# Optimization experiments

Measured on AMD Instinct MI355X. Metric: run time of the kernel, lower is better.

## Reference

```python
import jax, jax.numpy as jnp
import numpy as np

H, C, DK = 4, 63, 64   # n_head, context_size, d_k
NF = H * DK            # n_feat = 256


def setup_inputs() -> dict:
    key = jax.random.key(0)
    ks = jax.random.split(key, 7)
    B, T = 2, 4096
    query = jax.random.normal(ks[0], (B, T, NF), jnp.float32)
    key_t = jax.random.normal(ks[1], (B, T, NF), jnp.float32)   # dummy, unused
    value = jax.random.normal(ks[2], (B, T, NF), jnp.float32)
    mask = jnp.ones((B, 1, T), jnp.bool_)                       # dummy, unused
    s = 1.0 / np.sqrt(NF).astype(np.float32)
    w1 = jax.random.normal(ks[3], (NF, NF), jnp.float32) * s
    w2 = jax.random.normal(ks[4], (H * C, NF), jnp.float32) * s
    w3 = jax.random.normal(ks[5], (NF, NF), jnp.float32) * s
    w_out = jax.random.normal(ks[6], (NF, NF), jnp.float32) * s
    return {"query": query, "key": key_t, "value": value, "mask": mask,
            "w1": w1, "w2": w2, "w3": w3, "w_out": w_out}


def reference(query, key, value, mask, w1, w2, w3, w_out):
    # key and mask are dummies (unused), matching the original module.
    B, T, _ = query.shape
    half = (C - 1) // 2

    q = query @ w1.T                                            # (B,T,NF)
    # synthesized band scores: (B,H,T,C)
    weight = (jax.nn.relu(q) @ w2.T).reshape(B, T, H, C).transpose(0, 2, 1, 3)

    # band geometry: score(i, j) lives at offset k = j - i + half, |j-i| <= half
    j_idx = jnp.arange(T)[:, None] + jnp.arange(C)[None, :] - half   # (T,C)
    valid = (j_idx >= 0) & (j_idx < T)                               # (T,C)
    scores = jnp.where(valid[None, None], weight, -jnp.inf)
    p_attn = jax.nn.softmax(scores, axis=-1)                         # (B,H,T,C)

    v = (value @ w3.T).reshape(B, T, H, DK).transpose(0, 2, 1, 3)    # (B,H,T,DK)
    jc = jnp.clip(j_idx, 0, T - 1)                                   # safe gather idx
    windows = v[:, :, jc, :]                                         # (B,H,T,C,DK)
    x = jnp.einsum('bhtc,bhtcd->bhtd', p_attn, windows)              # (B,H,T,DK)

    x = x.transpose(0, 2, 1, 3).reshape(B, T, NF)
    return x @ w_out.T
```

## Files before the change

### kernel.cpp

```cpp
#include <hip/hip_runtime.h>
#include <hip/hip_bf16.h>
#include <math.h>

typedef _Float16 f16x8 __attribute__((ext_vector_type(8)));
typedef _Float16 f16x4 __attribute__((ext_vector_type(4)));
typedef float    f32x4 __attribute__((ext_vector_type(4)));

__device__ __host__ __forceinline__ int swz(int ch, int row) {
    return (ch & 24) | ((ch & 7) ^ (row & 7));
}
__device__ __forceinline__ f32x4 mfma16(f16x8 a, f16x8 b, f32x4 c) {
    return __builtin_amdgcn_mfma_f32_16x16x32_f16(a, b, c, 0, 0, 0);
}
__device__ __forceinline__ f16x8 cvt8(float4 lo, float4 hi) {
    f16x8 r = { (_Float16)lo.x, (_Float16)lo.y, (_Float16)lo.z, (_Float16)lo.w,
                (_Float16)hi.x, (_Float16)hi.y, (_Float16)hi.z, (_Float16)hi.w };
    return r;
}

__global__ __launch_bounds__(256) void convw(const float* __restrict__ w1,
                                             const float* __restrict__ w2,
                                             const float* __restrict__ w3,
                                             const float* __restrict__ wo,
                                             _Float16* __restrict__ p1,
                                             _Float16* __restrict__ p2,
                                             _Float16* __restrict__ p3,
                                             _Float16* __restrict__ po) {
    int gid = blockIdx.x * 256 + threadIdx.x;
    int widx = gid >> 13;
    int r    = gid & 8191;
    int lane = r & 63;
    int ks   = (r >> 6) & 7;
    int nblk = r >> 9;
    int n  = nblk * 16 + (lane & 15);
    int kc = (ks * 4 + (lane >> 4)) * 8;
    const float* src = widx == 0 ? w1 : widx == 1 ? w2 : widx == 2 ? w3 : wo;
    _Float16*    dst = widx == 0 ? p1 : widx == 1 ? p2 : widx == 2 ? p3 : po;
    f16x8 h = {};
    if (!(widx == 1 && n >= 252)) {
        float4 lo = *(const float4*)&src[n * 256 + kc];
        float4 hi = *(const float4*)&src[n * 256 + kc + 4];
        h = cvt8(lo, hi);
    }
    *(f16x8*)&dst[r * 8] = h;
}

__global__ __launch_bounds__(512, 2) void mono(const float* __restrict__ query,
                                               const float* __restrict__ value,
                                               const _Float16* __restrict__ w1p,
                                               const _Float16* __restrict__ w2p,
                                               const _Float16* __restrict__ w3p,
                                               const _Float16* __restrict__ wop,
                                               float* __restrict__ outp) {
    __shared__ __align__(16) _Float16 RA[16384];
    __shared__ __align__(16) _Float16 RB[8192];
    __shared__ __align__(16) _Float16 Vs[24576];
    __shared__ __align__(16) _Float16 vwT[26624];

    const int tid = threadIdx.x, lane = tid & 63, wid = tid >> 6;
    const int bidr = blockIdx.x;
    const int work = (bidr & 7) * 32 + (bidr >> 3);
    const int b   = work >> 7;
    const int t0  = (work & 127) * 32;
    const size_t rowb = (size_t)b * 4096;

    _Float16* Aq = RA;
    _Float16* Qr = RA + 8192;
    _Float16* Pl = RA;
    _Float16* sc = RB;
    _Float16* xb = RB;

    #pragma unroll
    for (int it = 0; it < 2; ++it) {
        int slot = it * 512 + tid;
        int row = slot >> 5, ch = slot & 31;
        const float* p = &query[(rowb + t0 + row) * 256 + ch * 8];
        float4 lo = *(const float4*)p, hi = *(const float4*)(p + 4);
        *(f16x8*)&Aq[row * 256 + swz(ch, row) * 8] = cvt8(lo, hi);
    }
    #pragma unroll
    for (int it = 0; it < 6; ++it) {
        int slot = it * 512 + tid;
        int row = slot >> 5, ch = slot & 31;
        int jl = t0 - 32 + row;
        jl = jl < 0 ? 0 : (jl > 4095 ? 4095 : jl);
        const float* p = &value[(rowb + jl) * 256 + ch * 8];
        float4 lo = *(const float4*)p, hi = *(const float4*)(p + 4);
        *(f16x8*)&Vs[row * 256 + swz(ch, row) * 8] = cvt8(lo, hi);
    }
    __syncthreads();

    {
        f32x4 acc[2][2] = {};
        #pragma unroll
        for (int ks = 0; ks < 8; ++ks) {
            int chn = ks * 4 + (lane >> 4);
            f16x8 af[2], bf[2];
            #pragma unroll
            for (int i = 0; i < 2; ++i) {
                int row = i * 16 + (lane & 15);
                af[i] = *(const f16x8*)&Aq[row * 256 + swz(chn, row) * 8];
            }
            #pragma unroll
            for (int j = 0; j < 2; ++j)
                bf[j] = *(const f16x8*)&w1p[(((wid * 2 + j) * 8 + ks) * 64 + lane) * 8];
            #pragma unroll
            for (int i = 0; i < 2; ++i)
                #pragma unroll
                for (int j = 0; j < 2; ++j)
                    acc[i][j] = mfma16(af[i], bf[j], acc[i][j]);
        }
        #pragma unroll
        for (int i = 0; i < 2; ++i)
            #pragma unroll
            for (int j = 0; j < 2; ++j)
                #pragma unroll
                for (int r = 0; r < 4; ++r) {
                    int row = i * 16 + ((lane >> 4) << 2) + r;
                    int n   = wid * 32 + j * 16 + (lane & 15);
                    float v = fmaxf(acc[i][j][r], 0.f);
                    Qr[row * 256 + swz(n >> 3, row) * 8 + (n & 7)] = (_Float16)v;
                }
    }
    __syncthreads();

    {
        f32x4 acc[2][2] = {};
        #pragma unroll
        for (int ks = 0; ks < 8; ++ks) {
            int chn = ks * 4 + (lane >> 4);
            f16x8 af[2], bf[2];
            #pragma unroll
            for (int i = 0; i < 2; ++i) {
                int row = i * 16 + (lane & 15);
                af[i] = *(const f16x8*)&Qr[row * 256 + swz(chn, row) * 8];
            }
            #pragma unroll
            for (int j = 0; j < 2; ++j)
                bf[j] = *(const f16x8*)&w2p[(((wid * 2 + j) * 8 + ks) * 64 + lane) * 8];
            #pragma unroll
            for (int i = 0; i < 2; ++i)
                #pragma unroll
                for (int j = 0; j < 2; ++j)
                    acc[i][j] = mfma16(af[i], bf[j], acc[i][j]);
        }
        #pragma unroll
        for (int i = 0; i < 2; ++i)
            #pragma unroll
            for (int j = 0; j < 2; ++j)
                #pragma unroll
                for (int r = 0; r < 4; ++r) {
                    int row = i * 16 + ((lane >> 4) << 2) + r;
                    int n   = wid * 32 + j * 16 + (lane & 15);
                    sc[row * 256 + n] = (_Float16)acc[i][j][r];
                }
    }

    {
        f32x4 a3[6][2] = {};
        #pragma unroll
        for (int ks = 0; ks < 8; ++ks) {
            int chn = ks * 4 + (lane >> 4);
            f16x8 bf[2];
            #pragma unroll
            for (int j = 0; j < 2; ++j)
                bf[j] = *(const f16x8*)&w3p[(((wid * 2 + j) * 8 + ks) * 64 + lane) * 8];
            #pragma unroll
            for (int mi = 0; mi < 6; ++mi) {
                int row = mi * 16 + (lane & 15);
                f16x8 af = *(const f16x8*)&Vs[row * 256 + swz(chn, row) * 8];
                #pragma unroll
                for (int j = 0; j < 2; ++j)
                    a3[mi][j] = mfma16(af, bf[j], a3[mi][j]);
            }
        }
        #pragma unroll
        for (int mi = 0; mi < 6; ++mi)
            #pragma unroll
            for (int j = 0; j < 2; ++j) {
                int d  = wid * 32 + j * 16 + (lane & 15);
                int jw = mi * 16 + ((lane >> 4) << 2);
                f16x4 h = { (_Float16)a3[mi][j][0], (_Float16)a3[mi][j][1],
                            (_Float16)a3[mi][j][2], (_Float16)a3[mi][j][3] };
                *(f16x4*)&vwT[d * 104 + jw] = h;
            }
    }
    __syncthreads();

    const int h = wid >> 1, half = wid & 1;
    #pragma unroll
    for (int it = 0; it < 4; ++it) {
        int s = it * 64 + lane;
        if (s < 208) {
            int rr = h * 32 + half * 16 + s / 13;
            int cc = s % 13;
            f16x8 z = {};
            *(f16x8*)&Pl[rr * 104 + cc * 8] = z;
        }
    }

    {
        const int hf = lane >> 5, c = lane & 31;
        #pragma unroll
        for (int i = 0; i < 8; ++i) {
            int tl = half * 16 + 2 * i + hf;
            int t  = t0 + tl;
            int c1 = c + 32;
            int j0 = t + c - 31, j1 = t + c1 - 31;
            bool ok0 = (j0 >= 0) && (j0 < 4096);
            bool ok1 = (c1 < 63) && (j1 >= 0) && (j1 < 4096);
            float s0 = ok0 ? (float)sc[tl * 256 + h * 63 + c]  : -INFINITY;
            float s1 = ok1 ? (float)sc[tl * 256 + h * 63 + c1] : -INFINITY;
            float mx = fmaxf(s0, s1);
            #pragma unroll
            for (int off = 16; off > 0; off >>= 1) mx = fmaxf(mx, __shfl_xor(mx, off));
            float e0 = ok0 ? __expf(s0 - mx) : 0.f;
            float e1 = ok1 ? __expf(s1 - mx) : 0.f;
            float sum = e0 + e1;
            #pragma unroll
            for (int off = 16; off > 0; off >>= 1) sum += __shfl_xor(sum, off);
            float inv = 1.0f / sum;
            Pl[(h * 32 + tl) * 104 + (tl + c + 1)] = (_Float16)(e0 * inv);
            if (c1 < 63) Pl[(h * 32 + tl) * 104 + (tl + c1 + 1)] = (_Float16)(e1 * inv);
        }
    }
    __syncthreads();

    {
        f32x4 xa[4] = {};
        #pragma unroll
        for (int ks = 0; ks < 3; ++ks) {
            int chn = ks * 4 + (lane >> 4);
            f16x8 af = *(const f16x8*)&Pl[(h * 32 + half * 16 + (lane & 15)) * 104 + chn * 8];
            #pragma unroll
            for (int j = 0; j < 4; ++j) {
                f16x8 bf = *(const f16x8*)&vwT[(h * 64 + j * 16 + (lane & 15)) * 104 + chn * 8];
                xa[j] = mfma16(af, bf, xa[j]);
            }
        }
        #pragma unroll
        for (int j = 0; j < 4; ++j)
            #pragma unroll
            for (int r = 0; r < 4; ++r) {
                int row = half * 16 + ((lane >> 4) << 2) + r;
                int n   = h * 64 + j * 16 + (lane & 15);
                xb[row * 256 + swz(n >> 3, row) * 8 + (n & 7)] = (_Float16)xa[j][r];
            }
    }
    __syncthreads();

    {
        f32x4 oa[2][2] = {};
        #pragma unroll
        for (int ks = 0; ks < 8; ++ks) {
            int chn = ks * 4 + (lane >> 4);
            f16x8 af[2], bf[2];
            #pragma unroll
            for (int i = 0; i < 2; ++i) {
                int row = i * 16 + (lane & 15);
                af[i] = *(const f16x8*)&xb[row * 256 + swz(chn, row) * 8];
            }
            #pragma unroll
            for (int j = 0; j < 2; ++j)
                bf[j] = *(const f16x8*)&wop[(((wid * 2 + j) * 8 + ks) * 64 + lane) * 8];
            #pragma unroll
            for (int i = 0; i < 2; ++i)
                #pragma unroll
                for (int j = 0; j < 2; ++j)
                    oa[i][j] = mfma16(af[i], bf[j], oa[i][j]);
        }
        #pragma unroll
        for (int i = 0; i < 2; ++i)
            #pragma unroll
            for (int j = 0; j < 2; ++j)
                #pragma unroll
                for (int r = 0; r < 4; ++r) {
                    int m = t0 + i * 16 + ((lane >> 4) << 2) + r;
                    int n = wid * 32 + j * 16 + (lane & 15);
                    outp[(rowb + m) * 256 + n] = oa[i][j][r];
                }
    }
}

extern "C" void kernel_launch(void* const* d_in, const int* in_sizes, int n_in,
                              void* d_out, int out_size, void* d_ws, size_t ws_size,
                              hipStream_t stream) {
    const float* query = (const float*)d_in[0];
    const float* value = (const float*)d_in[2];
    const float* w1    = (const float*)d_in[4];
    const float* w2    = (const float*)d_in[5];
    const float* w3    = (const float*)d_in[6];
    const float* w_out = (const float*)d_in[7];

    char* ws = (char*)d_ws;
    _Float16* w1p = (_Float16*)ws;
    _Float16* w2p = w1p + 65536;
    _Float16* w3p = w2p + 65536;
    _Float16* wop = w3p + 65536;

    convw<<<dim3(128), dim3(256), 0, stream>>>(w1, w2, w3, w_out, w1p, w2p, w3p, wop);
    mono<<<dim3(256), dim3(512), 0, stream>>>(query, value, w1p, w2p, w3p, wop, (float*)d_out);
}
```

Before: 28.63 us.

## Double block to 1024 threads and re-split every GEMM stage across 16 waves

Launches the fused kernel with 16 waves per block instead of 8 and redistributes every stage across the extra waves: the projection GEMMs, the V projection, the softmax rows and the banded PV product. Each wave now owns a 16-row by 32-column tile instead of 32 by 32. Because the large shared-memory footprint allows only one block per CU, this is meant to raise the number of resident waves and hide latency. The trade-off is less register-level reuse of A fragments, more redundant weight-fragment loads per block, and a higher per-thread register budget constraint.

```diff
diff --git a/kernel.cpp b/kernel.cpp
--- a/kernel.cpp
+++ b/kernel.cpp
@@ -45,13 +45,13 @@
     *(f16x8*)&dst[r * 8] = h;
 }
 
-__global__ __launch_bounds__(512, 2) void mono(const float* __restrict__ query,
-                                               const float* __restrict__ value,
-                                               const _Float16* __restrict__ w1p,
-                                               const _Float16* __restrict__ w2p,
-                                               const _Float16* __restrict__ w3p,
-                                               const _Float16* __restrict__ wop,
-                                               float* __restrict__ outp) {
+__global__ __launch_bounds__(1024) void mono(const float* __restrict__ query,
+                                             const float* __restrict__ value,
+                                             const _Float16* __restrict__ w1p,
+                                             const _Float16* __restrict__ w2p,
+                                             const _Float16* __restrict__ w3p,
+                                             const _Float16* __restrict__ wop,
+                                             float* __restrict__ outp) {
     __shared__ __align__(16) _Float16 RA[16384];
     __shared__ __align__(16) _Float16 RB[8192];
     __shared__ __align__(16) _Float16 Vs[24576];
@@ -70,17 +70,15 @@
     _Float16* sc = RB;
     _Float16* xb = RB;
 
-    #pragma unroll
-    for (int it = 0; it < 2; ++it) {
-        int slot = it * 512 + tid;
-        int row = slot >> 5, ch = slot & 31;
+    {
+        int row = tid >> 5, ch = tid & 31;
         const float* p = &query[(rowb + t0 + row) * 256 + ch * 8];
         float4 lo = *(const float4*)p, hi = *(const float4*)(p + 4);
         *(f16x8*)&Aq[row * 256 + swz(ch, row) * 8] = cvt8(lo, hi);
     }
     #pragma unroll
-    for (int it = 0; it < 6; ++it) {
-        int slot = it * 512 + tid;
+    for (int it = 0; it < 3; ++it) {
+        int slot = it * 1024 + tid;
         int row = slot >> 5, ch = slot & 31;
         int jl = t0 - 32 + row;
         jl = jl < 0 ? 0 : (jl > 4095 ? 4095 : jl);
@@ -90,84 +88,69 @@
     }
     __syncthreads();
 
-    {
-        f32x4 acc[2][2] = {};
-        #pragma unroll
-        for (int ks = 0; ks < 8; ++ks) {
-            int chn = ks * 4 + (lane >> 4);
-            f16x8 af[2], bf[2];
-            #pragma unroll
-            for (int i = 0; i < 2; ++i) {
-                int row = i * 16 + (lane & 15);
-                af[i] = *(const f16x8*)&Aq[row * 256 + swz(chn, row) * 8];
-            }
+    const int wm = wid >> 3;
+    const int wn = wid & 7;
+
+    {
+        f32x4 acc[2] = {};
+        #pragma unroll
+        for (int ks = 0; ks < 8; ++ks) {
+            int chn = ks * 4 + (lane >> 4);
+            int row = wm * 16 + (lane & 15);
+            f16x8 af = *(const f16x8*)&Aq[row * 256 + swz(chn, row) * 8];
+            #pragma unroll
+            for (int j = 0; j < 2; ++j) {
+                f16x8 bf = *(const f16x8*)&w1p[(((wn * 2 + j) * 8 + ks) * 64 + lane) * 8];
+                acc[j] = mfma16(af, bf, acc[j]);
+            }
+        }
+        #pragma unroll
+        for (int j = 0; j < 2; ++j)
+            #pragma unroll
+            for (int r = 0; r < 4; ++r) {
+                int row = wm * 16 + ((lane >> 4) << 2) + r;
+                int n   = wn * 32 + j * 16 + (lane & 15);
+                float v = fmaxf(acc[j][r], 0.f);
+                Qr[row * 256 + swz(n >> 3, row) * 8 + (n & 7)] = (_Float16)v;
+            }
+    }
+    __syncthreads();
+
+    {
+        f32x4 acc[2] = {};
+        #pragma unroll
+        for (int ks = 0; ks < 8; ++ks) {
+            int chn = ks * 4 + (lane >> 4);
+            int row = wm * 16 + (lane & 15);
+            f16x8 af = *(const f16x8*)&Qr[row * 256 + swz(chn, row) * 8];
+            #pragma unroll
+            for (int j = 0; j < 2; ++j) {
+                f16x8 bf = *(const f16x8*)&w2p[(((wn * 2 + j) * 8 + ks) * 64 + lane) * 8];
+                acc[j] = mfma16(af, bf, acc[j]);
+            }
+        }
+        #pragma unroll
+        for (int j = 0; j < 2; ++j)
+            #pragma unroll
+            for (int r = 0; r < 4; ++r) {
+                int row = wm * 16 + ((lane >> 4) << 2) + r;
+                int n   = wn * 32 + j * 16 + (lane & 15);
+                sc[row * 256 + n] = (_Float16)acc[j][r];
+            }
+    }
+
+    {
+        f32x4 a3[3][2] = {};
+        #pragma unroll
+        for (int ks = 0; ks < 8; ++ks) {
+            int chn = ks * 4 + (lane >> 4);
+            f16x8 bf[2];
             #pragma unroll
             for (int j = 0; j < 2; ++j)
-                bf[j] = *(const f16x8*)&w1p[(((wid * 2 + j) * 8 + ks) * 64 + lane) * 8];
-            #pragma unroll
-            for (int i = 0; i < 2; ++i)
-                #pragma unroll
-                for (int j = 0; j < 2; ++j)
-                    acc[i][j] = mfma16(af[i], bf[j], acc[i][j]);
-        }
-        #pragma unroll
-        for (int i = 0; i < 2; ++i)
-            #pragma unroll
-            for (int j = 0; j < 2; ++j)
-                #pragma unroll
-                for (int r = 0; r < 4; ++r) {
-                    int row = i * 16 + ((lane >> 4) << 2) + r;
-                    int n   = wid * 32 + j * 16 + (lane & 15);
-                    float v = fmaxf(acc[i][j][r], 0.f);
-                    Qr[row * 256 + swz(n >> 3, row) * 8 + (n & 7)] = (_Float16)v;
-                }
-    }
-    __syncthreads();
-
-    {
-        f32x4 acc[2][2] = {};
-        #pragma unroll
-        for (int ks = 0; ks < 8; ++ks) {
-            int chn = ks * 4 + (lane >> 4);
-            f16x8 af[2], bf[2];
-            #pragma unroll
-            for (int i = 0; i < 2; ++i) {
-                int row = i * 16 + (lane & 15);
-                af[i] = *(const f16x8*)&Qr[row * 256 + swz(chn, row) * 8];
-            }
-            #pragma unroll
-            for (int j = 0; j < 2; ++j)
-                bf[j] = *(const f16x8*)&w2p[(((wid * 2 + j) * 8 + ks) * 64 + lane) * 8];
-            #pragma unroll
-            for (int i = 0; i < 2; ++i)
-                #pragma unroll
-                for (int j = 0; j < 2; ++j)
-                    acc[i][j] = mfma16(af[i], bf[j], acc[i][j]);
-        }
-        #pragma unroll
-        for (int i = 0; i < 2; ++i)
-            #pragma unroll
-            for (int j = 0; j < 2; ++j)
-                #pragma unroll
-                for (int r = 0; r < 4; ++r) {
-                    int row = i * 16 + ((lane >> 4) << 2) + r;
-                    int n   = wid * 32 + j * 16 + (lane & 15);
-                    sc[row * 256 + n] = (_Float16)acc[i][j][r];
-                }
-    }
-
-    {
-        f32x4 a3[6][2] = {};
-        #pragma unroll
-        for (int ks = 0; ks < 8; ++ks) {
-            int chn = ks * 4 + (lane >> 4);
-            f16x8 bf[2];
-            #pragma unroll
-            for (int j = 0; j < 2; ++j)
-                bf[j] = *(const f16x8*)&w3p[(((wid * 2 + j) * 8 + ks) * 64 + lane) * 8];
-            #pragma unroll
-            for (int mi = 0; mi < 6; ++mi) {
-                int row = mi * 16 + (lane & 15);
+                bf[j] = *(const f16x8*)&w3p[(((wn * 2 + j) * 8 + ks) * 64 + lane) * 8];
+            #pragma unroll
+            for (int mi = 0; mi < 3; ++mi) {
+                int row = (wm * 3 + mi) * 16 + (lane & 15);
                 f16x8 af = *(const f16x8*)&Vs[row * 256 + swz(chn, row) * 8];
                 #pragma unroll
                 for (int j = 0; j < 2; ++j)
@@ -175,11 +158,11 @@
             }
         }
         #pragma unroll
-        for (int mi = 0; mi < 6; ++mi)
-            #pragma unroll
-            for (int j = 0; j < 2; ++j) {
-                int d  = wid * 32 + j * 16 + (lane & 15);
-                int jw = mi * 16 + ((lane >> 4) << 2);
+        for (int mi = 0; mi < 3; ++mi)
+            #pragma unroll
+            for (int j = 0; j < 2; ++j) {
+                int d  = wn * 32 + j * 16 + (lane & 15);
+                int jw = (wm * 3 + mi) * 16 + ((lane >> 4) << 2);
                 f16x4 h = { (_Float16)a3[mi][j][0], (_Float16)a3[mi][j][1],
                             (_Float16)a3[mi][j][2], (_Float16)a3[mi][j][3] };
                 *(f16x4*)&vwT[d * 104 + jw] = h;
@@ -187,12 +170,12 @@
     }
     __syncthreads();
 
-    const int h = wid >> 1, half = wid & 1;
+    const int h = wid >> 2, q = wid & 3;
     #pragma unroll
-    for (int it = 0; it < 4; ++it) {
+    for (int it = 0; it < 2; ++it) {
         int s = it * 64 + lane;
-        if (s < 208) {
-            int rr = h * 32 + half * 16 + s / 13;
+        if (s < 104) {
+            int rr = h * 32 + q * 8 + s / 13;
             int cc = s % 13;
             f16x8 z = {};
             *(f16x8*)&Pl[rr * 104 + cc * 8] = z;
@@ -202,8 +185,8 @@
     {
         const int hf = lane >> 5, c = lane & 31;
         #pragma unroll
-        for (int i = 0; i < 8; ++i) {
-            int tl = half * 16 + 2 * i + hf;
+        for (int i = 0; i < 4; ++i) {
+            int tl = q * 8 + 2 * i + hf;
             int t  = t0 + tl;
             int c1 = c + 32;
             int j0 = t + c - 31, j1 = t + c1 - 31;
@@ -227,58 +210,50 @@
     __syncthreads();
 
     {
-        f32x4 xa[4] = {};
+        const int th = (wid >> 1) & 1, dh = wid & 1;
+        f32x4 xa[2] = {};
         #pragma unroll
         for (int ks = 0; ks < 3; ++ks) {
             int chn = ks * 4 + (lane >> 4);
-            f16x8 af = *(const f16x8*)&Pl[(h * 32 + half * 16 + (lane & 15)) * 104 + chn * 8];
-            #pragma unroll
-            for (int j = 0; j < 4; ++j) {
-                f16x8 bf = *(const f16x8*)&vwT[(h * 64 + j * 16 + (lane & 15)) * 104 + chn * 8];
+            f16x8 af = *(const f16x8*)&Pl[(h * 32 + th * 16 + (lane & 15)) * 104 + chn * 8];
+            #pragma unroll
+            for (int j = 0; j < 2; ++j) {
+                f16x8 bf = *(const f16x8*)&vwT[(h * 64 + dh * 32 + j * 16 + (lane & 15)) * 104 + chn * 8];
                 xa[j] = mfma16(af, bf, xa[j]);
             }
         }
         #pragma unroll
-        for (int j = 0; j < 4; ++j)
-            #pragma unroll
-            for (int r = 0; r < 4; ++r) {
-                int row = half * 16 + ((lane >> 4) << 2) + r;
-                int n   = h * 64 + j * 16 + (lane & 15);
+        for (int j = 0; j < 2; ++j)
+            #pragma unroll
+            for (int r = 0; r < 4; ++r) {
+                int row = th * 16 + ((lane >> 4) << 2) + r;
+                int n   = h * 64 + dh * 32 + j * 16 + (lane & 15);
                 xb[row * 256 + swz(n >> 3, row) * 8 + (n & 7)] = (_Float16)xa[j][r];
             }
     }
     __syncthreads();
 
     {
-        f32x4 oa[2][2] = {};
-        #pragma unroll
-        for (int ks = 0; ks < 8; ++ks) {
-            int chn = ks * 4 + (lane >> 4);
-            f16x8 af[2], bf[2];
-            #pragma unroll
-            for (int i = 0; i < 2; ++i) {
-                int row = i * 16 + (lane & 15);
-                af[i] = *(const f16x8*)&xb[row * 256 + swz(chn, row) * 8];
-            }
-            #pragma unroll
-            for (int j = 0; j < 2; ++j)
-                bf[j] = *(const f16x8*)&wop[(((wid * 2 + j) * 8 + ks) * 64 + lane) * 8];
-            #pragma unroll
-            for (int i = 0; i < 2; ++i)
-                #pragma unroll
-                for (int j = 0; j < 2; ++j)
-                    oa[i][j] = mfma16(af[i], bf[j], oa[i][j]);
-        }
-        #pragma unroll
-        for (int i = 0; i < 2; ++i)
-            #pragma unroll
-            for (int j = 0; j < 2; ++j)
-                #pragma unroll
-                for (int r = 0; r < 4; ++r) {
-                    int m = t0 + i * 16 + ((lane >> 4) << 2) + r;
-                    int n = wid * 32 + j * 16 + (lane & 15);
-                    outp[(rowb + m) * 256 + n] = oa[i][j][r];
-                }
+        f32x4 oa[2] = {};
+        #pragma unroll
+        for (int ks = 0; ks < 8; ++ks) {
+            int chn = ks * 4 + (lane >> 4);
+            int row = wm * 16 + (lane & 15);
+            f16x8 af = *(const f16x8*)&xb[row * 256 + swz(chn, row) * 8];
+            #pragma unroll
+            for (int j = 0; j < 2; ++j) {
+                f16x8 bf = *(const f16x8*)&wop[(((wn * 2 + j) * 8 + ks) * 64 + lane) * 8];
+                oa[j] = mfma16(af, bf, oa[j]);
+            }
+        }
+        #pragma unroll
+        for (int j = 0; j < 2; ++j)
+            #pragma unroll
+            for (int r = 0; r < 4; ++r) {
+                int m = t0 + wm * 16 + ((lane >> 4) << 2) + r;
+                int n = wn * 32 + j * 16 + (lane & 15);
+                outp[(rowb + m) * 256 + n] = oa[j][r];
+            }
     }
 }
 
@@ -299,5 +274,5 @@
     _Float16* wop = w3p + 65536;
 
     convw<<<dim3(128), dim3(256), 0, stream>>>(w1, w2, w3, w_out, w1p, w2p, w3p, wop);
-    mono<<<dim3(256), dim3(512), 0, stream>>>(query, value, w1p, w2p, w3p, wop, (float*)d_out);
-}
+    mono<<<dim3(256), dim3(1024), 0, stream>>>(query, value, w1p, w2p, w3p, wop, (float*)d_out);
+}
```

New measurement: 28.69 us. About the same (+0.2%).
